# Performance work log

Measured on AMD Instinct MI355X. Metric: run time of the kernel, lower is better.

The kernel has to match this reference:

```python
import jax, jax.numpy as jnp
import numpy as np

N, E, F_IN, EDGE_DIM = 50000, 800000, 128, 64
H, C = 4, 64  # heads, per-head out channels
NEG_SLOPE = 0.2  # PyG GATConv default


def setup_inputs() -> dict:
    key = jax.random.key(0)
    ks = jax.random.split(key, 16)
    p = lambda i, shape: jax.random.normal(ks[i], shape, jnp.float32) * 0.05
    return {
        "node_features": jax.random.normal(ks[0], (N, F_IN), jnp.float32),
        "edge_features": jax.random.normal(ks[1], (E, EDGE_DIM), jnp.float32),
        "edge_index": jax.random.randint(ks[2], (2, E), 0, N),
        # layer 1 (concat=True, ELU)
        "W1": p(3, (F_IN, H * C)),
        "att_src1": p(4, (H, C)), "att_dst1": p(5, (H, C)), "att_edge1": p(6, (H, C)),
        "bias1": jnp.zeros((H * C,), jnp.float32),
        "edgeW1": p(7, (EDGE_DIM, H * C)),
        # layer 2 (concat=False -> mean over heads, no activation)
        "W2": p(8, (H * C, H * C)),
        "att_src2": p(9, (H, C)), "att_dst2": p(10, (H, C)), "att_edge2": p(11, (H, C)),
        "bias2": jnp.zeros((C,), jnp.float32),
        "edgeW2": p(12, (EDGE_DIM, H * C)),
    }


def _gat_layer(x, edge_feat, src, dst, W, a_s, a_d, a_e, bias, edgeW, concat):
    n = x.shape[0]
    h = (x @ W).reshape(n, H, C)                      # [N,H,C]
    ef = (edge_feat @ edgeW).reshape(-1, H, C)        # [E,H,C] edge_linear projection
    # GATConv add_self_loops=True, fill_value='mean': self-loop attr = mean of incoming edge attrs
    ones = jnp.ones((src.shape[0],), x.dtype)
    cnt = jnp.maximum(jax.ops.segment_sum(ones, dst, num_segments=n), 1.0)
    loop_attr = jax.ops.segment_sum(ef, dst, num_segments=n) / cnt[:, None, None]
    ef_f = jnp.concatenate([ef, loop_attr], axis=0)   # [E+N,H,C]
    loops = jnp.arange(n)
    src_f = jnp.concatenate([src, loops], axis=0)
    dst_f = jnp.concatenate([dst, loops], axis=0)
    # per-edge attention logits: alpha_j + alpha_i + alpha_edge
    a_src = jnp.einsum('nhc,hc->nh', h, a_s)
    a_dst = jnp.einsum('nhc,hc->nh', h, a_d)
    logits = a_src[src_f] + a_dst[dst_f] + jnp.einsum('ehc,hc->eh', ef_f, a_e)
    logits = jax.nn.leaky_relu(logits, NEG_SLOPE)     # [E+N,H]
    # segment softmax over incoming edges of each dst node (every node has a self-loop)
    m = jax.ops.segment_max(logits, dst_f, num_segments=n)
    pexp = jnp.exp(logits - m[dst_f])
    denom = jax.ops.segment_sum(pexp, dst_f, num_segments=n)
    alpha = pexp / (denom[dst_f] + 1e-16)
    # message = x_j * alpha, scatter-add to dst
    out = jax.ops.segment_sum(h[src_f] * alpha[..., None], dst_f, num_segments=n)  # [N,H,C]
    if concat:
        return out.reshape(n, H * C) + bias
    return out.mean(axis=1) + bias


def reference(node_features, edge_features, edge_index,
              W1, att_src1, att_dst1, att_edge1, bias1, edgeW1,
              W2, att_src2, att_dst2, att_edge2, bias2, edgeW2):
    src, dst = edge_index[0], edge_index[1]
    x = _gat_layer(node_features, edge_features, src, dst,
                   W1, att_src1, att_dst1, att_edge1, bias1, edgeW1, concat=True)
    x = jax.nn.elu(x)
    return _gat_layer(x, edge_features, src, dst,
                      W2, att_src2, att_dst2, att_edge2, bias2, edgeW2, concat=False)
```

## Files before the change

### kernel.cpp

```cpp
#include <hip/hip_runtime.h>
#include <hip/hip_fp16.h>
#include <math.h>

#define NNODE 50000
#define NEDGE 800000
#define FIN 128
#define EDIM 64
#define HC 256
#define NH 4
#define CC 64
#define SCAN_TILE 512
#define EB 128

typedef _Float16 half8v __attribute__((ext_vector_type(8)));
typedef _Float16 half4v __attribute__((ext_vector_type(4)));
typedef float floatx4 __attribute__((ext_vector_type(4)));

__global__ void k_count(const int* __restrict__ dst, int* counts, int E) {
    int e = blockIdx.x * 256 + threadIdx.x;
    if (e < E) atomicAdd(&counts[dst[e]], 1);
}

__global__ void k_scan1(const int* __restrict__ counts, int* offs, int* tilesums, int N) {
    __shared__ int s[SCAN_TILE];
    int t = threadIdx.x;
    int i = blockIdx.x * SCAN_TILE + t;
    int v = (i < N) ? counts[i] : 0;
    s[t] = v;
    for (int off = 1; off < SCAN_TILE; off <<= 1) {
        __syncthreads();
        int x = (t >= off) ? s[t - off] : 0;
        __syncthreads();
        s[t] += x;
    }
    __syncthreads();
    if (i < N) offs[i] = s[t] - v;
    if (t == SCAN_TILE - 1) tilesums[blockIdx.x] = s[t];
}

__global__ void k_scan2(int* tilesums, int nt) {
    if (threadIdx.x == 0) {
        int run = 0;
        for (int i = 0; i < nt; i++) { int v = tilesums[i]; tilesums[i] = run; run += v; }
    }
}

__global__ void k_scan3(int* offs, const int* __restrict__ tilesums, int N, int E) {
    int t = threadIdx.x;
    int i = blockIdx.x * SCAN_TILE + t;
    if (i < N) offs[i] += tilesums[blockIdx.x];
    if (i == 0) offs[N] = E;
}

__global__ void k_fill(const int* __restrict__ src, const int* __restrict__ dst,
                       const int* __restrict__ offs, int* cursor,
                       int2* __restrict__ es, int E) {
    int e = blockIdx.x * 256 + threadIdx.x;
    if (e < E) {
        int d = dst[e];
        int pos = offs[d] + atomicAdd(&cursor[d], 1);
        es[pos] = make_int2(e, src[e]);
    }
}

__device__ inline float4 h4_to_f4(uint2 r) {
    float2 fa = __half22float2(*(__half2*)&r.x);
    float2 fb = __half22float2(*(__half2*)&r.y);
    return make_float4(fa.x, fa.y, fb.x, fb.y);
}

__device__ inline float sel_h(float4 v, int head) {
    return head == 0 ? v.x : head == 1 ? v.y : head == 2 ? v.z : v.w;
}

__global__ void k_castW(const float* __restrict__ W, _Float16* __restrict__ Wt, int K) {
    int k = blockIdx.x, n = threadIdx.x;
    Wt[(size_t)n * K + k] = (_Float16)W[(size_t)k * HC + n];
}

template <typename AT>
__global__ __launch_bounds__(256) void k_gemm_mfma(const AT* __restrict__ A,
                                                   const _Float16* __restrict__ Wt16,
                                                   _Float16* __restrict__ H16,
                                                   const float* __restrict__ att_s,
                                                   const float* __restrict__ att_d,
                                                   float* __restrict__ asrc,
                                                   float* __restrict__ adst,
                                                   int M, int K) {
    int wave = threadIdx.x >> 6, lane = threadIdx.x & 63;
    int quad = lane >> 4, l16 = lane & 15;
    int row = blockIdx.x * 64 + wave * 16 + l16;
    bool rok = row < M;
    floatx4 acc[16];
#pragma unroll
    for (int i = 0; i < 16; i++) acc[i] = (floatx4)(0.0f);
    int nk = K >> 5;
    for (int kk = 0; kk < nk; kk++) {
        half8v a = {};
        if (rok) {
            if constexpr (sizeof(AT) == 2) {
                a = *(const half8v*)(A + (size_t)row * K + kk * 32 + quad * 8);
            } else {
                const float* ap = (const float*)A + (size_t)row * K + kk * 32 + quad * 8;
                float4 v0 = *(const float4*)ap;
                float4 v1 = *(const float4*)(ap + 4);
                a[0] = (_Float16)v0.x; a[1] = (_Float16)v0.y;
                a[2] = (_Float16)v0.z; a[3] = (_Float16)v0.w;
                a[4] = (_Float16)v1.x; a[5] = (_Float16)v1.y;
                a[6] = (_Float16)v1.z; a[7] = (_Float16)v1.w;
            }
        }
#pragma unroll
        for (int nt = 0; nt < 16; nt++) {
            half8v b = *(const half8v*)(Wt16 + (size_t)(nt * 16 + l16) * K + kk * 32 + quad * 8);
            acc[nt] = __builtin_amdgcn_mfma_f32_16x16x32_f16(a, b, acc[nt], 0, 0, 0);
        }
    }
    float asl[16], adl[16];
#pragma unroll
    for (int nt = 0; nt < 16; nt++) {
        asl[nt] = att_s[nt * 16 + l16];
        adl[nt] = att_d[nt * 16 + l16];
    }
    int orow0 = blockIdx.x * 64 + wave * 16 + quad * 4;
#pragma unroll
    for (int r = 0; r < 4; r++) {
        int orow = orow0 + r;
        float4 vs4, vd4;
        float* vsp = (float*)&vs4;
        float* vdp = (float*)&vd4;
#pragma unroll
        for (int hh = 0; hh < 4; hh++) {
            float vs = 0.f, vd = 0.f;
#pragma unroll
            for (int q = 0; q < 4; q++) {
                int nt = hh * 4 + q;
                float hv = acc[nt][r];
                vs += hv * asl[nt];
                vd += hv * adl[nt];
            }
            vs += __shfl_xor(vs, 1, 64); vd += __shfl_xor(vd, 1, 64);
            vs += __shfl_xor(vs, 2, 64); vd += __shfl_xor(vd, 2, 64);
            vs += __shfl_xor(vs, 4, 64); vd += __shfl_xor(vd, 4, 64);
            vs += __shfl_xor(vs, 8, 64); vd += __shfl_xor(vd, 8, 64);
            vsp[hh] = vs; vdp[hh] = vd;
        }
        if (l16 == 0 && orow < M) {
            ((float4*)asrc)[orow] = vs4;
            ((float4*)adst)[orow] = vd4;
        }
    }
#pragma unroll
    for (int r = 0; r < 4; r++) {
        int orow = orow0 + r;
        if (orow < M) {
#pragma unroll
            for (int nt = 0; nt < 16; nt++)
                H16[(size_t)orow * HC + nt * 16 + l16] = (_Float16)acc[nt][r];
        }
    }
}

__global__ void k_weatt(const float* __restrict__ edgeW, const float* __restrict__ att_e,
                        float* we) {
    int t = threadIdx.x;
    int d = t >> 2, hh = t & 3;
    float s = 0.f;
    for (int c = 0; c < 64; c++) s += edgeW[d * HC + hh * 64 + c] * att_e[hh * 64 + c];
    we[d * 4 + hh] = s;
}

__global__ __launch_bounds__(128) void k_elog_both(const float* __restrict__ ef,
                                                   const float* __restrict__ we1,
                                                   const float* __restrict__ we2,
                                                   float* __restrict__ elog1,
                                                   float* __restrict__ elog2, int E) {
    __shared__ float sEf[EB][65];
    int t = threadIdx.x;
    int e0 = blockIdx.x * EB;
    for (int i = 0; i < 16; i++) {
        int q = t + i * 128;
        int le = q >> 4, c4 = (q & 15) << 2;
        int ge = e0 + le;
        float4 v = make_float4(0.f, 0.f, 0.f, 0.f);
        if (ge < E) v = *(const float4*)(ef + (size_t)ge * EDIM + c4);
        sEf[le][c4 + 0] = v.x; sEf[le][c4 + 1] = v.y;
        sEf[le][c4 + 2] = v.z; sEf[le][c4 + 3] = v.w;
    }
    __syncthreads();
    float a1[4] = {}, a2[4] = {};
#pragma unroll 8
    for (int c = 0; c < 64; c++) {
        float v = sEf[t][c];
        float4 w1 = *(const float4*)(we1 + c * 4);
        float4 w2 = *(const float4*)(we2 + c * 4);
        a1[0] += v * w1.x; a1[1] += v * w1.y; a1[2] += v * w1.z; a1[3] += v * w1.w;
        a2[0] += v * w2.x; a2[1] += v * w2.y; a2[2] += v * w2.z; a2[3] += v * w2.w;
    }
    int e = e0 + t;
    if (e < E) {
        ((float4*)elog1)[e] = make_float4(a1[0], a1[1], a1[2], a1[3]);
        ((float4*)elog2)[e] = make_float4(a2[0], a2[1], a2[2], a2[3]);
    }
}

__global__ __launch_bounds__(256) void k_pedge(const float* __restrict__ elog,
                                               const float* __restrict__ asrc,
                                               const float* __restrict__ adst,
                                               const int* __restrict__ offs,
                                               const int2* __restrict__ es,
                                               float* __restrict__ pcsr,
                                               float* __restrict__ pself, int N) {
    int wave = threadIdx.x >> 6, lane = threadIdx.x & 63;
    int n = blockIdx.x * 4 + wave;
    if (n >= N) return;
    int beg = offs[n], end = offs[n + 1];
    float4 adn = ((const float4*)adst)[n];
    float s0 = 0.f, s1 = 0.f, s2 = 0.f, s3 = 0.f;
    for (int i0 = beg; i0 < end; i0 += 64) {
        int i = i0 + lane;
        if (i < end) {
            int2 e = es[i];
            float4 el = ((const float4*)elog)[e.x];
            float4 as4 = ((const float4*)asrc)[e.y];
            s0 += el.x; s1 += el.y; s2 += el.z; s3 += el.w;
            float4 o;
            float l;
            l = as4.x + adn.x + el.x; l = l > 0.f ? l : 0.2f * l; o.x = expf(l);
            l = as4.y + adn.y + el.y; l = l > 0.f ? l : 0.2f * l; o.y = expf(l);
            l = as4.z + adn.z + el.z; l = l > 0.f ? l : 0.2f * l; o.z = expf(l);
            l = as4.w + adn.w + el.w; l = l > 0.f ? l : 0.2f * l; o.w = expf(l);
            ((float4*)pcsr)[i] = o;
        }
    }
    for (int m = 32; m >= 1; m >>= 1) {
        s0 += __shfl_xor(s0, m, 64);
        s1 += __shfl_xor(s1, m, 64);
        s2 += __shfl_xor(s2, m, 64);
        s3 += __shfl_xor(s3, m, 64);
    }
    if (lane == 0) {
        float cnt = (float)(end - beg);
        if (cnt < 1.f) cnt = 1.f;
        float4 asn = ((const float4*)asrc)[n];
        float4 o;
        float l;
        l = asn.x + adn.x + s0 / cnt; l = l > 0.f ? l : 0.2f * l; o.x = expf(l);
        l = asn.y + adn.y + s1 / cnt; l = l > 0.f ? l : 0.2f * l; o.y = expf(l);
        l = asn.z + adn.z + s2 / cnt; l = l > 0.f ? l : 0.2f * l; o.z = expf(l);
        l = asn.w + adn.w + s3 / cnt; l = l > 0.f ? l : 0.2f * l; o.w = expf(l);
        ((float4*)pself)[n] = o;
    }
}

template <int LAYER>
__global__ __launch_bounds__(256) void k_aggr(const _Float16* __restrict__ hb,
                                              const float* __restrict__ pcsr,
                                              const float* __restrict__ pself,
                                              const int* __restrict__ offs,
                                              const int2* __restrict__ es,
                                              const float* __restrict__ bias,
                                              _Float16* __restrict__ out16,
                                              float* __restrict__ out32, int N) {
    int wave = threadIdx.x >> 6, lane = threadIdx.x & 63;
    int n = blockIdx.x * 4 + wave;
    if (n >= N) return;
    int head = lane >> 4;
    const uint2* hf = (const uint2*)hb;
    const float4* pc = (const float4*)pcsr;
    int beg = offs[n], end = offs[n + 1];

    float4 ps4 = ((const float4*)pself)[n];
    float ps = sel_h(ps4, head);
    float4 hv = h4_to_f4(hf[(size_t)n * 64 + lane]);
    float denom = ps;
    float ax = ps * hv.x, ay = ps * hv.y, az = ps * hv.z, aw = ps * hv.w;

    int i = beg;
    for (; i + 8 <= end; i += 8) {
        int s[8];
        uint2 r[8];
        float4 p[8];
#pragma unroll
        for (int j = 0; j < 8; j++) s[j] = es[i + j].y;
#pragma unroll
        for (int j = 0; j < 8; j++) r[j] = hf[(size_t)s[j] * 64 + lane];
#pragma unroll
        for (int j = 0; j < 8; j++) p[j] = pc[i + j];
#pragma unroll
        for (int j = 0; j < 8; j++) {
            float w = sel_h(p[j], head);
            float4 h4 = h4_to_f4(r[j]);
            denom += w;
            ax += w * h4.x; ay += w * h4.y; az += w * h4.z; aw += w * h4.w;
        }
    }
    for (; i < end; i++) {
        int s0 = es[i].y;
        float4 p0 = pc[i];
        float4 h4 = h4_to_f4(hf[(size_t)s0 * 64 + lane]);
        float w0 = sel_h(p0, head);
        denom += w0;
        ax += w0 * h4.x; ay += w0 * h4.y; az += w0 * h4.z; aw += w0 * h4.w;
    }
    float inv = 1.0f / (denom + 1e-16f);
    ax *= inv; ay *= inv; az *= inv; aw *= inv;

    if (LAYER == 1) {
        float4 bv = ((const float4*)bias)[lane];
        half4v o;
        float v;
        v = ax + bv.x; o[0] = (_Float16)(v > 0.f ? v : expf(v) - 1.0f);
        v = ay + bv.y; o[1] = (_Float16)(v > 0.f ? v : expf(v) - 1.0f);
        v = az + bv.z; o[2] = (_Float16)(v > 0.f ? v : expf(v) - 1.0f);
        v = aw + bv.w; o[3] = (_Float16)(v > 0.f ? v : expf(v) - 1.0f);
        ((half4v*)(out16 + (size_t)n * HC))[lane] = o;
    } else {
        ax += __shfl_xor(ax, 16, 64); ax += __shfl_xor(ax, 32, 64);
        ay += __shfl_xor(ay, 16, 64); ay += __shfl_xor(ay, 32, 64);
        az += __shfl_xor(az, 16, 64); az += __shfl_xor(az, 32, 64);
        aw += __shfl_xor(aw, 16, 64); aw += __shfl_xor(aw, 32, 64);
        if (lane < 16) {
            float4 bv = ((const float4*)bias)[lane];
            float4 o;
            o.x = 0.25f * ax + bv.x;
            o.y = 0.25f * ay + bv.y;
            o.z = 0.25f * az + bv.z;
            o.w = 0.25f * aw + bv.w;
            ((float4*)(out32 + (size_t)n * CC))[lane] = o;
        }
    }
}

extern "C" void kernel_launch(void* const* d_in, const int* in_sizes, int n_in,
                              void* d_out, int out_size, void* d_ws, size_t ws_size,
                              hipStream_t stream) {
    const float* x   = (const float*)d_in[0];
    const float* ef  = (const float*)d_in[1];
    const int*   ei  = (const int*)d_in[2];
    const float* W1  = (const float*)d_in[3];
    const float* as1 = (const float*)d_in[4];
    const float* ad1 = (const float*)d_in[5];
    const float* ae1 = (const float*)d_in[6];
    const float* b1  = (const float*)d_in[7];
    const float* eW1 = (const float*)d_in[8];
    const float* W2  = (const float*)d_in[9];
    const float* as2 = (const float*)d_in[10];
    const float* ad2 = (const float*)d_in[11];
    const float* ae2 = (const float*)d_in[12];
    const float* b2  = (const float*)d_in[13];
    const float* eW2 = (const float*)d_in[14];
    float* out = (float*)d_out;
    const int* srcp = ei;
    const int* dstp = ei + NEDGE;

    char* w = (char*)d_ws;
    auto alloc = [&](size_t bytes) -> char* {
        char* r = w;
        w += (bytes + 255) / 256 * 256;
        return r;
    };
    _Float16* hb16  = (_Float16*)alloc((size_t)NNODE * HC * 2);
    _Float16* x216  = (_Float16*)alloc((size_t)NNODE * HC * 2);
    _Float16* wt1   = (_Float16*)alloc((size_t)HC * FIN * 2);
    _Float16* wt2   = (_Float16*)alloc((size_t)HC * HC * 2);
    float* elog1  = (float*)alloc((size_t)NEDGE * 4 * 4);
    float* elog2  = (float*)alloc((size_t)NEDGE * 4 * 4);
    float* pbuf   = (float*)alloc((size_t)NEDGE * 4 * 4);
    float* asrc   = (float*)alloc((size_t)NNODE * 4 * 4);
    float* adst   = (float*)alloc((size_t)NNODE * 4 * 4);
    float* pself  = (float*)alloc((size_t)NNODE * 4 * 4);
    float* webuf1 = (float*)alloc(64 * 4 * 4);
    float* webuf2 = (float*)alloc(64 * 4 * 4);
    int* counts  = (int*)alloc((size_t)NNODE * 4);
    int* offs    = (int*)alloc((size_t)(NNODE + 1) * 4);
    int* tiles   = (int*)alloc(1024 * 4);
    int* cursor  = (int*)alloc((size_t)NNODE * 4);
    int2* es     = (int2*)alloc((size_t)NEDGE * 8);

    hipMemsetAsync(counts, 0, (size_t)NNODE * 4, stream);
    hipMemsetAsync(cursor, 0, (size_t)NNODE * 4, stream);

    k_count<<<(NEDGE + 255) / 256, 256, 0, stream>>>(dstp, counts, NEDGE);
    int nt = (NNODE + SCAN_TILE - 1) / SCAN_TILE;
    k_scan1<<<nt, SCAN_TILE, 0, stream>>>(counts, offs, tiles, NNODE);
    k_scan2<<<1, 64, 0, stream>>>(tiles, nt);
    k_scan3<<<nt, SCAN_TILE, 0, stream>>>(offs, tiles, NNODE, NEDGE);
    k_fill<<<(NEDGE + 255) / 256, 256, 0, stream>>>(srcp, dstp, offs, cursor, es, NEDGE);

    k_castW<<<FIN, 256, 0, stream>>>(W1, wt1, FIN);
    k_castW<<<HC, 256, 0, stream>>>(W2, wt2, HC);

    k_weatt<<<1, 256, 0, stream>>>(eW1, ae1, webuf1);
    k_weatt<<<1, 256, 0, stream>>>(eW2, ae2, webuf2);
    k_elog_both<<<(NEDGE + EB - 1) / EB, EB, 0, stream>>>(ef, webuf1, webuf2, elog1, elog2, NEDGE);

    k_gemm_mfma<float><<<(NNODE + 63) / 64, 256, 0, stream>>>(x, wt1, hb16, as1, ad1, asrc, adst, NNODE, FIN);
    k_pedge<<<(NNODE + 3) / 4, 256, 0, stream>>>(elog1, asrc, adst, offs, es, pbuf, pself, NNODE);
    k_aggr<1><<<(NNODE + 3) / 4, 256, 0, stream>>>(hb16, pbuf, pself, offs, es, b1, x216, nullptr, NNODE);

    k_gemm_mfma<_Float16><<<(NNODE + 63) / 64, 256, 0, stream>>>(x216, wt2, hb16, as2, ad2, asrc, adst, NNODE, HC);
    k_pedge<<<(NNODE + 3) / 4, 256, 0, stream>>>(elog2, asrc, adst, offs, es, pbuf, pself, NNODE);
    k_aggr<2><<<(NNODE + 3) / 4, 256, 0, stream>>>(hb16, pbuf, pself, offs, es, b2, nullptr, out, NNODE);
}
```

Before: 805.5 us.

## Fuse edge softmax weights into aggregation and store edge logits in CSR order

Removes the separate per-edge kernel that computed exp weights into a buffer. Aggregation now recomputes leaky-relu/exp logits inline from CSR-ordered edge logits and source attention scores, then folds in the self-loop term at the end. The fill kernel now writes split src arrays and an edge-to-CSR-position map, so the edge-logit kernel scatters directly into CSR order and later loads are contiguous. The single-thread tile scan becomes a parallel shared-memory scan. In exchange, every head lane repeats the exp work, and the edge-logit writes become scattered.

```diff
diff --git a/kernel.cpp b/kernel.cpp
--- a/kernel.cpp
+++ b/kernel.cpp
@@ -39,10 +39,18 @@
 }
 
 __global__ void k_scan2(int* tilesums, int nt) {
-    if (threadIdx.x == 0) {
-        int run = 0;
-        for (int i = 0; i < nt; i++) { int v = tilesums[i]; tilesums[i] = run; run += v; }
-    }
+    __shared__ int s[128];
+    int t = threadIdx.x;
+    int v = (t < nt) ? tilesums[t] : 0;
+    s[t] = v;
+    for (int off = 1; off < 128; off <<= 1) {
+        __syncthreads();
+        int x = (t >= off) ? s[t - off] : 0;
+        __syncthreads();
+        s[t] += x;
+    }
+    __syncthreads();
+    if (t < nt) tilesums[t] = s[t] - v;
 }
 
 __global__ void k_scan3(int* offs, const int* __restrict__ tilesums, int N, int E) {
@@ -54,12 +62,13 @@
 
 __global__ void k_fill(const int* __restrict__ src, const int* __restrict__ dst,
                        const int* __restrict__ offs, int* cursor,
-                       int2* __restrict__ es, int E) {
+                       int* __restrict__ srcs, int* __restrict__ epos, int E) {
     int e = blockIdx.x * 256 + threadIdx.x;
     if (e < E) {
         int d = dst[e];
         int pos = offs[d] + atomicAdd(&cursor[d], 1);
-        es[pos] = make_int2(e, src[e]);
+        srcs[pos] = src[e];
+        epos[e] = pos;
     }
 }
 
@@ -173,8 +182,9 @@
 __global__ __launch_bounds__(128) void k_elog_both(const float* __restrict__ ef,
                                                    const float* __restrict__ we1,
                                                    const float* __restrict__ we2,
-                                                   float* __restrict__ elog1,
-                                                   float* __restrict__ elog2, int E) {
+                                                   const int* __restrict__ epos,
+                                                   float* __restrict__ elogc1,
+                                                   float* __restrict__ elogc2, int E) {
     __shared__ float sEf[EB][65];
     int t = threadIdx.x;
     int e0 = blockIdx.x * EB;
@@ -199,110 +209,87 @@
     }
     int e = e0 + t;
     if (e < E) {
-        ((float4*)elog1)[e] = make_float4(a1[0], a1[1], a1[2], a1[3]);
-        ((float4*)elog2)[e] = make_float4(a2[0], a2[1], a2[2], a2[3]);
-    }
-}
-
-__global__ __launch_bounds__(256) void k_pedge(const float* __restrict__ elog,
-                                               const float* __restrict__ asrc,
-                                               const float* __restrict__ adst,
-                                               const int* __restrict__ offs,
-                                               const int2* __restrict__ es,
-                                               float* __restrict__ pcsr,
-                                               float* __restrict__ pself, int N) {
-    int wave = threadIdx.x >> 6, lane = threadIdx.x & 63;
-    int n = blockIdx.x * 4 + wave;
-    if (n >= N) return;
-    int beg = offs[n], end = offs[n + 1];
-    float4 adn = ((const float4*)adst)[n];
-    float s0 = 0.f, s1 = 0.f, s2 = 0.f, s3 = 0.f;
-    for (int i0 = beg; i0 < end; i0 += 64) {
-        int i = i0 + lane;
-        if (i < end) {
-            int2 e = es[i];
-            float4 el = ((const float4*)elog)[e.x];
-            float4 as4 = ((const float4*)asrc)[e.y];
-            s0 += el.x; s1 += el.y; s2 += el.z; s3 += el.w;
-            float4 o;
-            float l;
-            l = as4.x + adn.x + el.x; l = l > 0.f ? l : 0.2f * l; o.x = expf(l);
-            l = as4.y + adn.y + el.y; l = l > 0.f ? l : 0.2f * l; o.y = expf(l);
-            l = as4.z + adn.z + el.z; l = l > 0.f ? l : 0.2f * l; o.z = expf(l);
-            l = as4.w + adn.w + el.w; l = l > 0.f ? l : 0.2f * l; o.w = expf(l);
-            ((float4*)pcsr)[i] = o;
-        }
-    }
-    for (int m = 32; m >= 1; m >>= 1) {
-        s0 += __shfl_xor(s0, m, 64);
-        s1 += __shfl_xor(s1, m, 64);
-        s2 += __shfl_xor(s2, m, 64);
-        s3 += __shfl_xor(s3, m, 64);
-    }
-    if (lane == 0) {
-        float cnt = (float)(end - beg);
-        if (cnt < 1.f) cnt = 1.f;
-        float4 asn = ((const float4*)asrc)[n];
-        float4 o;
-        float l;
-        l = asn.x + adn.x + s0 / cnt; l = l > 0.f ? l : 0.2f * l; o.x = expf(l);
-        l = asn.y + adn.y + s1 / cnt; l = l > 0.f ? l : 0.2f * l; o.y = expf(l);
-        l = asn.z + adn.z + s2 / cnt; l = l > 0.f ? l : 0.2f * l; o.z = expf(l);
-        l = asn.w + adn.w + s3 / cnt; l = l > 0.f ? l : 0.2f * l; o.w = expf(l);
-        ((float4*)pself)[n] = o;
+        int pos = epos[e];
+        ((float4*)elogc1)[pos] = make_float4(a1[0], a1[1], a1[2], a1[3]);
+        ((float4*)elogc2)[pos] = make_float4(a2[0], a2[1], a2[2], a2[3]);
     }
 }
 
 template <int LAYER>
-__global__ __launch_bounds__(256) void k_aggr(const _Float16* __restrict__ hb,
-                                              const float* __restrict__ pcsr,
-                                              const float* __restrict__ pself,
-                                              const int* __restrict__ offs,
-                                              const int2* __restrict__ es,
-                                              const float* __restrict__ bias,
-                                              _Float16* __restrict__ out16,
-                                              float* __restrict__ out32, int N) {
+__global__ __launch_bounds__(256) void k_aggr_fused(const _Float16* __restrict__ hb,
+                                                    const float* __restrict__ elogc,
+                                                    const float* __restrict__ asrc,
+                                                    const float* __restrict__ adst,
+                                                    const int* __restrict__ offs,
+                                                    const int* __restrict__ srcs,
+                                                    const float* __restrict__ bias,
+                                                    _Float16* __restrict__ out16,
+                                                    float* __restrict__ out32, int N) {
     int wave = threadIdx.x >> 6, lane = threadIdx.x & 63;
     int n = blockIdx.x * 4 + wave;
     if (n >= N) return;
     int head = lane >> 4;
     const uint2* hf = (const uint2*)hb;
-    const float4* pc = (const float4*)pcsr;
+    const float4* elc = (const float4*)elogc;
+    const float4* asp = (const float4*)asrc;
     int beg = offs[n], end = offs[n + 1];
 
-    float4 ps4 = ((const float4*)pself)[n];
-    float ps = sel_h(ps4, head);
-    float4 hv = h4_to_f4(hf[(size_t)n * 64 + lane]);
-    float denom = ps;
-    float ax = ps * hv.x, ay = ps * hv.y, az = ps * hv.z, aw = ps * hv.w;
+    float adnh = sel_h(((const float4*)adst)[n], head);
+    float asnh = sel_h(asp[n], head);
+
+    float denom = 0.f, selsum = 0.f;
+    float ax = 0.f, ay = 0.f, az = 0.f, aw = 0.f;
 
     int i = beg;
     for (; i + 8 <= end; i += 8) {
         int s[8];
         uint2 r[8];
-        float4 p[8];
-#pragma unroll
-        for (int j = 0; j < 8; j++) s[j] = es[i + j].y;
+        float4 el[8];
+        float4 a4[8];
+#pragma unroll
+        for (int j = 0; j < 8; j++) s[j] = srcs[i + j];
 #pragma unroll
         for (int j = 0; j < 8; j++) r[j] = hf[(size_t)s[j] * 64 + lane];
 #pragma unroll
-        for (int j = 0; j < 8; j++) p[j] = pc[i + j];
+        for (int j = 0; j < 8; j++) el[j] = elc[i + j];
+#pragma unroll
+        for (int j = 0; j < 8; j++) a4[j] = asp[s[j]];
 #pragma unroll
         for (int j = 0; j < 8; j++) {
-            float w = sel_h(p[j], head);
+            float eh = sel_h(el[j], head);
+            selsum += eh;
+            float l = sel_h(a4[j], head) + adnh + eh;
+            l = l > 0.f ? l : 0.2f * l;
+            float w = expf(l);
+            denom += w;
             float4 h4 = h4_to_f4(r[j]);
-            denom += w;
             ax += w * h4.x; ay += w * h4.y; az += w * h4.z; aw += w * h4.w;
         }
     }
     for (; i < end; i++) {
-        int s0 = es[i].y;
-        float4 p0 = pc[i];
-        float4 h4 = h4_to_f4(hf[(size_t)s0 * 64 + lane]);
-        float w0 = sel_h(p0, head);
-        denom += w0;
-        ax += w0 * h4.x; ay += w0 * h4.y; az += w0 * h4.z; aw += w0 * h4.w;
-    }
+        int s0 = srcs[i];
+        uint2 r0 = hf[(size_t)s0 * 64 + lane];
+        float4 el0 = elc[i];
+        float4 a40 = asp[s0];
+        float eh = sel_h(el0, head);
+        selsum += eh;
+        float l = sel_h(a40, head) + adnh + eh;
+        l = l > 0.f ? l : 0.2f * l;
+        float w = expf(l);
+        denom += w;
+        float4 h4 = h4_to_f4(r0);
+        ax += w * h4.x; ay += w * h4.y; az += w * h4.z; aw += w * h4.w;
+    }
+
+    float cnt = (float)(end - beg);
+    if (cnt < 1.f) cnt = 1.f;
+    float ls = asnh + adnh + selsum / cnt;
+    ls = ls > 0.f ? ls : 0.2f * ls;
+    float ws = expf(ls);
+    denom += ws;
+    float4 hn = h4_to_f4(hf[(size_t)n * 64 + lane]);
+    ax += ws * hn.x; ay += ws * hn.y; az += ws * hn.z; aw += ws * hn.w;
+
     float inv = 1.0f / (denom + 1e-16f);
     ax *= inv; ay *= inv; az *= inv; aw *= inv;
 
@@ -364,19 +351,18 @@
     _Float16* x216  = (_Float16*)alloc((size_t)NNODE * HC * 2);
     _Float16* wt1   = (_Float16*)alloc((size_t)HC * FIN * 2);
     _Float16* wt2   = (_Float16*)alloc((size_t)HC * HC * 2);
-    float* elog1  = (float*)alloc((size_t)NEDGE * 4 * 4);
-    float* elog2  = (float*)alloc((size_t)NEDGE * 4 * 4);
-    float* pbuf   = (float*)alloc((size_t)NEDGE * 4 * 4);
+    float* elogc1 = (float*)alloc((size_t)NEDGE * 4 * 4);
+    float* elogc2 = (float*)alloc((size_t)NEDGE * 4 * 4);
     float* asrc   = (float*)alloc((size_t)NNODE * 4 * 4);
     float* adst   = (float*)alloc((size_t)NNODE * 4 * 4);
-    float* pself  = (float*)alloc((size_t)NNODE * 4 * 4);
     float* webuf1 = (float*)alloc(64 * 4 * 4);
     float* webuf2 = (float*)alloc(64 * 4 * 4);
     int* counts  = (int*)alloc((size_t)NNODE * 4);
     int* offs    = (int*)alloc((size_t)(NNODE + 1) * 4);
     int* tiles   = (int*)alloc(1024 * 4);
     int* cursor  = (int*)alloc((size_t)NNODE * 4);
-    int2* es     = (int2*)alloc((size_t)NEDGE * 8);
+    int* srcs    = (int*)alloc((size_t)NEDGE * 4);
+    int* epos    = (int*)alloc((size_t)NEDGE * 4);
 
     hipMemsetAsync(counts, 0, (size_t)NNODE * 4, stream);
     hipMemsetAsync(cursor, 0, (size_t)NNODE * 4, stream);
@@ -384,22 +370,20 @@
     k_count<<<(NEDGE + 255) / 256, 256, 0, stream>>>(dstp, counts, NEDGE);
     int nt = (NNODE + SCAN_TILE - 1) / SCAN_TILE;
     k_scan1<<<nt, SCAN_TILE, 0, stream>>>(counts, offs, tiles, NNODE);
-    k_scan2<<<1, 64, 0, stream>>>(tiles, nt);
+    k_scan2<<<1, 128, 0, stream>>>(tiles, nt);
     k_scan3<<<nt, SCAN_TILE, 0, stream>>>(offs, tiles, NNODE, NEDGE);
-    k_fill<<<(NEDGE + 255) / 256, 256, 0, stream>>>(srcp, dstp, offs, cursor, es, NEDGE);
+    k_fill<<<(NEDGE + 255) / 256, 256, 0, stream>>>(srcp, dstp, offs, cursor, srcs, epos, NEDGE);
 
     k_castW<<<FIN, 256, 0, stream>>>(W1, wt1, FIN);
     k_castW<<<HC, 256, 0, stream>>>(W2, wt2, HC);
 
     k_weatt<<<1, 256, 0, stream>>>(eW1, ae1, webuf1);
     k_weatt<<<1, 256, 0, stream>>>(eW2, ae2, webuf2);
-    k_elog_both<<<(NEDGE + EB - 1) / EB, EB, 0, stream>>>(ef, webuf1, webuf2, elog1, elog2, NEDGE);
+    k_elog_both<<<(NEDGE + EB - 1) / EB, EB, 0, stream>>>(ef, webuf1, webuf2, epos, elogc1, elogc2, NEDGE);
 
     k_gemm_mfma<float><<<(NNODE + 63) / 64, 256, 0, stream>>>(x, wt1, hb16, as1, ad1, asrc, adst, NNODE, FIN);
-    k_pedge<<<(NNODE + 3) / 4, 256, 0, stream>>>(elog1, asrc, adst, offs, es, pbuf, pself, NNODE);
-    k_aggr<1><<<(NNODE + 3) / 4, 256, 0, stream>>>(hb16, pbuf, pself, offs, es, b1, x216, nullptr, NNODE);
+    k_aggr_fused<1><<<(NNODE + 3) / 4, 256, 0, stream>>>(hb16, elogc1, asrc, adst, offs, srcs, b1, x216, nullptr, NNODE);
 
     k_gemm_mfma<_Float16><<<(NNODE + 63) / 64, 256, 0, stream>>>(x216, wt2, hb16, as2, ad2, asrc, adst, NNODE, HC);
-    k_pedge<<<(NNODE + 3) / 4, 256, 0, stream>>>(elog2, asrc, adst, offs, es, pbuf, pself, NNODE);
-    k_aggr<2><<<(NNODE + 3) / 4, 256, 0, stream>>>(hb16, pbuf, pself, offs, es, b2, nullptr, out, NNODE);
-}
+    k_aggr_fused<2><<<(NNODE + 3) / 4, 256, 0, stream>>>(hb16, elogc2, asrc, adst, offs, srcs, b2, nullptr, out, NNODE);
+}
```

New measurement: 880.7 us. 1.09x slower.
